# Optimization experiments

Hardware: AMD Instinct MI355X
Metric: run time of the kernel (lower is better)

Reference implementation:

```python
import jax, jax.numpy as jnp
import numpy as np

N = 100000   # total nodes
E = 1000000  # edges
D = 64       # input_dim
H = 128      # embed_dim


def setup_inputs() -> dict:
    key = jax.random.key(0)
    k1, k2, k3, k4 = jax.random.split(key, 4)
    nodes = jnp.arange(N, dtype=jnp.int32)
    features = jax.random.normal(k1, (N, D), dtype=jnp.float32)
    edge_index = jax.random.randint(k2, (2, E), 0, N, dtype=jnp.int32)
    # nn.Linear(2*D, H): weight [H, 2D], bias [H]
    W = jax.random.normal(k3, (H, 2 * D), dtype=jnp.float32) / np.sqrt(2 * D)
    b = jax.random.normal(k4, (H,), dtype=jnp.float32) * 0.01
    return {"nodes": nodes, "features": features, "edge_index": edge_index,
            "W": W, "b": b}


def reference(nodes, features, edge_index, W, b):
    src, dst = edge_index[0], edge_index[1]
    # gcn=False: neighbors are undirected (both src->dst and dst->src).
    # Mean aggregator over all neighbors (full-neighborhood mean).
    ones = jnp.ones((E,), dtype=features.dtype)
    neigh_sum = (jax.ops.segment_sum(features[dst], src, num_segments=N)
                 + jax.ops.segment_sum(features[src], dst, num_segments=N))
    deg = (jax.ops.segment_sum(ones, src, num_segments=N)
           + jax.ops.segment_sum(ones, dst, num_segments=N))
    neigh_mean = neigh_sum / jnp.maximum(deg, 1.0)[:, None]  # [N, D]
    self_feats = features[nodes]            # [B, D]
    neigh_feats = neigh_mean[nodes]         # [B, D]
    combined = jnp.concatenate([self_feats, neigh_feats], axis=1)  # [B, 2D]
    out = jax.nn.relu(combined @ W.T + b)   # [B, H]
    return out
```

## Files before the change

### kernel.cpp

```cpp
#include <hip/hip_runtime.h>
#include <hip/hip_bf16.h>


#define D_IN 64
#define H_OUT 128
#define CAP 64
#define CAP_L 61
#define NPB 32
#define BSHIFT 7
#define BUK_N 128
#define NBUK_MAX 1024
#define PASSA_BLOCKS 256
#define PASSA_THREADS 512

typedef unsigned long long ull;
typedef unsigned short ushortt;
typedef unsigned char uchar;
typedef __attribute__((ext_vector_type(8))) short bf16x8;
typedef __attribute__((ext_vector_type(4))) float f32x4;
typedef __attribute__((ext_vector_type(2))) float f32x2;

__device__ __forceinline__ ushortt f2bf(float f) {
    __hip_bfloat16 h = __float2bfloat16(f);
    return *reinterpret_cast<ushortt*>(&h);
}
__device__ __forceinline__ float bf2f(ushortt u) {
    unsigned int x = ((unsigned int)u) << 16;
    return __uint_as_float(x);
}

__global__ __launch_bounds__(PASSA_THREADS) void prep_kernel(
    const int* __restrict__ ei,
    unsigned* __restrict__ gbuf,
    int* __restrict__ blkcnt,
    const float4* __restrict__ feat4,
    const float4* __restrict__ w4,
    ushortt* __restrict__ fb,
    uint2* __restrict__ fq,
    ushortt* __restrict__ Wb,
    int E, int nbuk, int scap, int chunk, int nfeat8, int nw8)
{
    const int t = threadIdx.x;

    if (blockIdx.x >= PASSA_BLOCKS) {
        int i = (blockIdx.x - PASSA_BLOCKS) * PASSA_THREADS + t;
        if (i < nfeat8) {
            float4 a = feat4[2 * i], b = feat4[2 * i + 1];
            bf16x8 o;
            o[0] = (short)f2bf(a.x); o[1] = (short)f2bf(a.y);
            o[2] = (short)f2bf(a.z); o[3] = (short)f2bf(a.w);
            o[4] = (short)f2bf(b.x); o[5] = (short)f2bf(b.y);
            o[6] = (short)f2bf(b.z); o[7] = (short)f2bf(b.w);
            *(bf16x8*)&fb[(size_t)i * 8] = o;
            unsigned lo = (unsigned)__builtin_amdgcn_cvt_pk_fp8_f32(a.x, a.y, 0, false);
            lo = (unsigned)__builtin_amdgcn_cvt_pk_fp8_f32(a.z, a.w, (int)lo, true);
            unsigned hi = (unsigned)__builtin_amdgcn_cvt_pk_fp8_f32(b.x, b.y, 0, false);
            hi = (unsigned)__builtin_amdgcn_cvt_pk_fp8_f32(b.z, b.w, (int)hi, true);
            uint2 q; q.x = lo; q.y = hi;
            fq[i] = q;
        } else {
            int j = i - nfeat8;
            if (j < nw8) {
                float4 a = w4[2 * j], b = w4[2 * j + 1];
                bf16x8 o;
                o[0] = (short)f2bf(a.x); o[1] = (short)f2bf(a.y);
                o[2] = (short)f2bf(a.z); o[3] = (short)f2bf(a.w);
                o[4] = (short)f2bf(b.x); o[5] = (short)f2bf(b.y);
                o[6] = (short)f2bf(b.z); o[7] = (short)f2bf(b.w);
                *(bf16x8*)&Wb[(size_t)j * 8] = o;
            }
        }
        return;
    }

    __shared__ int lcnt[NBUK_MAX];
    for (int i = t; i < nbuk; i += PASSA_THREADS) lcnt[i] = 0;
    __syncthreads();

    const int E2 = 2 * E;
    int lo = blockIdx.x * chunk;
    int hi = lo + chunk; if (hi > E2) hi = E2;

    for (int i = lo + t; i < hi; i += PASSA_THREADS) {
        int u = ei[i];
        int v = (i < E) ? ei[E + i] : ei[i - E];
        int b = u >> BSHIFT;
        unsigned pk = ((unsigned)v << BSHIFT) | (unsigned)(u & (BUK_N - 1));
        int p = atomicAdd(&lcnt[b], 1);
        if (p < scap) gbuf[((size_t)blockIdx.x * nbuk + b) * scap + p] = pk;
    }
    __syncthreads();
    for (int b = t; b < nbuk; b += PASSA_THREADS)
        blkcnt[blockIdx.x * nbuk + b] = lcnt[b];
}

__global__ __launch_bounds__(512, 8) void adj_agg_kernel(
    const unsigned* __restrict__ gbuf,
    const int* __restrict__ blkcnt,
    const int* __restrict__ ei,
    const uchar* __restrict__ fq,
    ushortt* __restrict__ meanb,
    int N, int E, int nbuk, int scap)
{
    __shared__ unsigned adj_l[BUK_N * CAP_L];
    __shared__ int cnt_l[BUK_N];
    __shared__ int scnt_l[PASSA_BLOCKS];
    __shared__ int satf;

    const int b = blockIdx.x;
    const int t = threadIdx.x;

    if (t == 0) satf = 0;
    if (t < BUK_N) cnt_l[t] = 0;
    if (t < PASSA_BLOCKS) {
        int c = blkcnt[t * nbuk + b];
        scnt_l[t] = c;
        if (c > scap) satf = 1;
    }
    __syncthreads();

    const int wv   = t >> 6;
    const int lane = t & 63;

    if (satf) {
        const int E2 = 2 * E;
        for (int i = t; i < E2; i += 512) {
            int u = ei[i];
            if ((u >> BSHIFT) != b) continue;
            int v = (i < E) ? ei[E + i] : ei[i - E];
            int ul = u & (BUK_N - 1);
            int p  = atomicAdd(&cnt_l[ul], 1);
            if (p < CAP_L) adj_l[ul * CAP_L + p] = (unsigned)v;
        }
    } else {
        for (int seg = wv; seg < PASSA_BLOCKS; seg += 8) {
            int c = scnt_l[seg]; if (c > scap) c = scap;
            const unsigned* base = gbuf + ((size_t)seg * nbuk + b) * scap;
            for (int i = lane; i < c; i += 64) {
                unsigned e = base[i];
                int ul = e & (BUK_N - 1);
                int v  = (int)(e >> BSHIFT);
                int p  = atomicAdd(&cnt_l[ul], 1);
                if (p < CAP_L) adj_l[ul * CAP_L + p] = (unsigned)v;
            }
        }
    }
    __syncthreads();

    const int oct = lane >> 3;
    const int ol  = lane & 7;
    const uchar* fqb = fq + ol * 8;

    const int nbase = wv * 16;
    const int gbase = (b << BSHIFT) + nbase;

#define GATHER(U0, U1, U2, U3, AROW, CC)                                     \
    {                                                                        \
        if ((CC) > 0) {                                                      \
            int jj = oct;      int a = jj < (CC);                            \
            unsigned id = (AROW)[a ? jj : 0];                                \
            U0 = *(const uint2*)(fqb + (size_t)(id * 64u));                  \
            if (!a) { U0.x = 0u; U0.y = 0u; }                                \
        } else { U0.x = 0u; U0.y = 0u; }                                     \
        if ((CC) > 8) {                                                      \
            int jj = 8 + oct;  int a = jj < (CC);                            \
            unsigned id = (AROW)[a ? jj : 0];                                \
            U1 = *(const uint2*)(fqb + (size_t)(id * 64u));                  \
            if (!a) { U1.x = 0u; U1.y = 0u; }                                \
        } else { U1.x = 0u; U1.y = 0u; }                                     \
        if ((CC) > 16) {                                                     \
            int jj = 16 + oct; int a = jj < (CC);                            \
            unsigned id = (AROW)[a ? jj : 0];                                \
            U2 = *(const uint2*)(fqb + (size_t)(id * 64u));                  \
            if (!a) { U2.x = 0u; U2.y = 0u; }                                \
        } else { U2.x = 0u; U2.y = 0u; }                                     \
        if ((CC) > 24) {                                                     \
            int jj = 24 + oct; int a = jj < (CC);                            \
            unsigned id = (AROW)[a ? jj : 0];                                \
            U3 = *(const uint2*)(fqb + (size_t)(id * 64u));                  \
            if (!a) { U3.x = 0u; U3.y = 0u; }                                \
        } else { U3.x = 0u; U3.y = 0u; }                                     \
    }

#define DEC(u)                                                       \
    s0 += __builtin_amdgcn_cvt_pk_f32_fp8((int)(u).x, false);        \
    s1 += __builtin_amdgcn_cvt_pk_f32_fp8((int)(u).x, true);         \
    s2 += __builtin_amdgcn_cvt_pk_f32_fp8((int)(u).y, false);        \
    s3 += __builtin_amdgcn_cvt_pk_f32_fp8((int)(u).y, true);

    uint2 cu0, cu1, cu2, cu3;
    uint2 nu0, nu1, nu2, nu3;

    int c_cur = 0, cc_cur = 0;
    {
        if (gbase < N) c_cur = cnt_l[nbase];
        cc_cur = c_cur < CAP_L ? c_cur : CAP_L;
        const unsigned* arow = &adj_l[nbase * CAP_L];
        GATHER(cu0, cu1, cu2, cu3, arow, cc_cur);
    }

    for (int ni = 0; ni < 16; ++ni) {
        const int n = nbase + ni;
        const int g = gbase + ni;

        int c_nxt = 0, cc_nxt = 0;
        if (ni < 15) {
            if (g + 1 < N) c_nxt = cnt_l[n + 1];
            cc_nxt = c_nxt < CAP_L ? c_nxt : CAP_L;
            const unsigned* arown = &adj_l[(n + 1) * CAP_L];
            GATHER(nu0, nu1, nu2, nu3, arown, cc_nxt);
        }

        if (g < N) {
            f32x2 s0 = {0.f, 0.f}, s1 = {0.f, 0.f};
            f32x2 s2 = {0.f, 0.f}, s3 = {0.f, 0.f};
            DEC(cu0); DEC(cu1); DEC(cu2); DEC(cu3);

            if (__builtin_expect(cc_cur > 32, 0)) {
                const unsigned* arow = &adj_l[n * CAP_L];
                for (int j = 32; j < cc_cur; j += 8) {
                    int jj = j + oct; int a = jj < cc_cur;
                    unsigned id = arow[a ? jj : 0];
                    uint2 u = *(const uint2*)(fqb + (size_t)(id * 64u));
                    if (!a) { u.x = 0u; u.y = 0u; }
                    DEC(u);
                }
            }

            f32x2 a0, a1;
            {
                f32x2 t0, t1, t2, t3;
                t0.x = __shfl_xor(s0.x, 8);  t0.y = __shfl_xor(s0.y, 8);
                t1.x = __shfl_xor(s1.x, 8);  t1.y = __shfl_xor(s1.y, 8);
                t2.x = __shfl_xor(s2.x, 8);  t2.y = __shfl_xor(s2.y, 8);
                t3.x = __shfl_xor(s3.x, 8);  t3.y = __shfl_xor(s3.y, 8);
                bool hi = (oct & 1);
                a0 = hi ? (s2 + t2) : (s0 + t0);
                a1 = hi ? (s3 + t3) : (s1 + t1);
            }
            f32x2 b0;
            {
                f32x2 t0, t1;
                t0.x = __shfl_xor(a0.x, 16); t0.y = __shfl_xor(a0.y, 16);
                t1.x = __shfl_xor(a1.x, 16); t1.y = __shfl_xor(a1.y, 16);
                bool hi = (oct & 2);
                b0 = hi ? (a1 + t1) : (a0 + t0);
            }
            float cf;
            {
                f32x2 tt;
                tt.x = __shfl_xor(b0.x, 32); tt.y = __shfl_xor(b0.y, 32);
                f32x2 ss = b0 + tt;
                cf = (oct & 4) ? ss.y : ss.x;
            }

            float r = 1.0f / fmaxf((float)c_cur, 1.0f);
            int d = 8 * ol + 4 * (oct & 1) + (oct & 2) + ((oct >> 2) & 1);
            meanb[(size_t)g * D_IN + d] = f2bf(cf * r);
        }

        c_cur = c_nxt; cc_cur = cc_nxt;
        cu0 = nu0; cu1 = nu1; cu2 = nu2; cu3 = nu3;
    }
#undef GATHER
#undef DEC
}

__global__ __launch_bounds__(256) void build_adj_kernel(
    const int* __restrict__ ei,
    int* __restrict__ cnt,
    int* __restrict__ adj,
    int E)
{
    const int part   = blockIdx.x & 7;
    const int bloc   = blockIdx.x >> 3;
    const int nbp    = gridDim.x >> 3;
    const int stride = nbp * 256;
    const int E2     = 2 * E;

    for (int i = bloc * 256 + (int)threadIdx.x; i < E2; i += stride) {
        int u = ei[i];
        if (((u >> 4) & 7) != part) continue;
        int v = (i < E) ? ei[E + i] : ei[i - E];
        int p = atomicAdd(&cnt[u], 1);
        if (p < CAP_L) adj[u * CAP + p] = v;
    }
}

__global__ __launch_bounds__(256) void aggregate_f32_kernel(
    const float* __restrict__ feat,
    const int* __restrict__ adj,
    const int* __restrict__ cnt,
    ushortt* __restrict__ meanb,
    int N)
{
    int wid  = (blockIdx.x * blockDim.x + threadIdx.x) >> 6;
    int lane = threadIdx.x & 63;
    if (wid >= N) return;

    int c  = cnt[wid];
    int cc = c < CAP_L ? c : CAP_L;
    int ids = adj[wid * CAP + lane];

    float sum = 0.0f;
    int j = 0;
    for (; j + 8 <= cc; j += 8) {
        int i0 = __shfl(ids, j + 0);
        int i1 = __shfl(ids, j + 1);
        int i2 = __shfl(ids, j + 2);
        int i3 = __shfl(ids, j + 3);
        int i4 = __shfl(ids, j + 4);
        int i5 = __shfl(ids, j + 5);
        int i6 = __shfl(ids, j + 6);
        int i7 = __shfl(ids, j + 7);
        float f0 = feat[i0 * D_IN + lane];
        float f1 = feat[i1 * D_IN + lane];
        float f2 = feat[i2 * D_IN + lane];
        float f3 = feat[i3 * D_IN + lane];
        float f4 = feat[i4 * D_IN + lane];
        float f5 = feat[i5 * D_IN + lane];
        float f6 = feat[i6 * D_IN + lane];
        float f7 = feat[i7 * D_IN + lane];
        sum += ((f0 + f1) + (f2 + f3)) + ((f4 + f5) + (f6 + f7));
    }
    for (; j < cc; ++j)
        sum += feat[__shfl(ids, j) * D_IN + lane];

    float m = sum / fmaxf((float)c, 1.0f);
    meanb[(size_t)wid * D_IN + lane] = f2bf(m);
}

__global__ __launch_bounds__(256) void gemm_mfma_kernel(
    const int* __restrict__ nodes,
    const ushortt* __restrict__ fb,
    const ushortt* __restrict__ meanb,
    const ushortt* __restrict__ Wb,
    const float* __restrict__ bias,
    float* __restrict__ out,
    int N)
{
    __shared__ ushortt w_lds[128 * 136];
    __shared__ int gnode[64];

    const int t  = threadIdx.x;
    const int n0 = blockIdx.x * 64;

    if (t < 64) {
        int idx = n0 + t;
        gnode[t] = nodes[idx < N ? idx : N - 1];
    }
    for (int i = t; i < 128 * 16; i += 256) {
        int row = i >> 4, seg = i & 15;
        *(bf16x8*)&w_lds[row * 136 + seg * 8] =
            *(const bf16x8*)&Wb[row * 128 + seg * 8];
    }
    __syncthreads();

    const int w    = t >> 6;
    const int lane = t & 63;
    const int l15  = lane & 15;
    const int quad = lane >> 4;

    const int g = gnode[w * 16 + l15];
    const bf16x8 a0 = *(const bf16x8*)&fb[(size_t)g * D_IN +  0 + quad * 8];
    const bf16x8 a1 = *(const bf16x8*)&fb[(size_t)g * D_IN + 32 + quad * 8];
    const bf16x8 a2 = *(const bf16x8*)&meanb[(size_t)g * D_IN +  0 + quad * 8];
    const bf16x8 a3 = *(const bf16x8*)&meanb[(size_t)g * D_IN + 32 + quad * 8];

    const int  out_row = n0 + w * 16 + l15;
    const bool valid   = out_row < N;

#pragma unroll
    for (int tile = 0; tile < 8; ++tile) {
        const int h0 = tile * 16;
        const ushortt* wrow = &w_lds[(h0 + l15) * 136];
        bf16x8 b0 = *(const bf16x8*)&wrow[ 0 + quad * 8];
        bf16x8 b1 = *(const bf16x8*)&wrow[32 + quad * 8];
        bf16x8 b2 = *(const bf16x8*)&wrow[64 + quad * 8];
        bf16x8 b3 = *(const bf16x8*)&wrow[96 + quad * 8];

        f32x4 acc = {0.f, 0.f, 0.f, 0.f};
        acc = __builtin_amdgcn_mfma_f32_16x16x32_bf16(b0, a0, acc, 0, 0, 0);
        acc = __builtin_amdgcn_mfma_f32_16x16x32_bf16(b1, a1, acc, 0, 0, 0);
        acc = __builtin_amdgcn_mfma_f32_16x16x32_bf16(b2, a2, acc, 0, 0, 0);
        acc = __builtin_amdgcn_mfma_f32_16x16x32_bf16(b3, a3, acc, 0, 0, 0);

        if (valid) {
            float4 bv = *(const float4*)&bias[h0 + quad * 4];
            float4 o;
            o.x = fmaxf(acc[0] + bv.x, 0.0f);
            o.y = fmaxf(acc[1] + bv.y, 0.0f);
            o.z = fmaxf(acc[2] + bv.z, 0.0f);
            o.w = fmaxf(acc[3] + bv.w, 0.0f);
            *(float4*)&out[(size_t)out_row * H_OUT + h0 + quad * 4] = o;
        }
    }
}

__global__ __launch_bounds__(256) void gemm_kernel(
    const int* __restrict__ nodes,
    const float* __restrict__ feat,
    const ushortt* __restrict__ meanb,
    const float* __restrict__ W,
    const float* __restrict__ bias,
    float* __restrict__ out,
    int N)
{
    __shared__ float w_lds[64 * 132];
    __shared__ float comb_self[NPB * 68];
    __shared__ float comb_mean[NPB * 68];
    __shared__ int   gnode[NPB];

    const int t  = threadIdx.x;
    const int n0 = blockIdx.x * NPB;

    if (t < NPB) {
        int idx = n0 + t;
        if (idx >= N) idx = N - 1;
        gnode[t] = nodes[idx];
    }
    __syncthreads();

    for (int i = t; i < NPB * 64; i += 256) {
        int n = i >> 6, d = i & 63;
        int g = gnode[n];
        comb_self[n * 68 + d] = feat[g * D_IN + d];
        comb_mean[n * 68 + d] = bf2f(meanb[(size_t)g * D_IN + d]);
    }
    for (int i = t; i < H_OUT * 64; i += 256) {
        int h = i >> 6, kk = i & 63;
        w_lds[kk * 132 + h] = W[h * (2 * D_IN) + kk];
    }
    __syncthreads();

    const int tx = t & 31;
    const int ty = t >> 5;
    const int h0 = tx * 4;
    const int nl = ty * 4;

    float acc[4][4];
#pragma unroll
    for (int j = 0; j < 4; j++)
#pragma unroll
        for (int i = 0; i < 4; i++) acc[j][i] = 0.0f;

    for (int kk = 0; kk < 64; kk += 4) {
        float4 wvv[4], cv[4];
#pragma unroll
        for (int i = 0; i < 4; i++)
            wvv[i] = *(const float4*)&w_lds[(kk + i) * 132 + h0];
#pragma unroll
        for (int j = 0; j < 4; j++)
            cv[j] = *(const float4*)&comb_self[(nl + j) * 68 + kk];
#pragma unroll
        for (int j = 0; j < 4; j++) {
            const float* c = (const float*)&cv[j];
#pragma unroll
            for (int i = 0; i < 4; i++) {
                const float* wp = (const float*)&wvv[i];
                acc[j][0] += wp[0] * c[i];
                acc[j][1] += wp[1] * c[i];
                acc[j][2] += wp[2] * c[i];
                acc[j][3] += wp[3] * c[i];
            }
        }
    }
    __syncthreads();

    for (int i = t; i < H_OUT * 64; i += 256) {
        int h = i >> 6, kk = i & 63;
        w_lds[kk * 132 + h] = W[h * (2 * D_IN) + 64 + kk];
    }
    __syncthreads();

    for (int kk = 0; kk < 64; kk += 4) {
        float4 wvv[4], cv[4];
#pragma unroll
        for (int i = 0; i < 4; i++)
            wvv[i] = *(const float4*)&w_lds[(kk + i) * 132 + h0];
#pragma unroll
        for (int j = 0; j < 4; j++)
            cv[j] = *(const float4*)&comb_mean[(nl + j) * 68 + kk];
#pragma unroll
        for (int j = 0; j < 4; j++) {
            const float* c = (const float*)&cv[j];
#pragma unroll
            for (int i = 0; i < 4; i++) {
                const float* wp = (const float*)&wvv[i];
                acc[j][0] += wp[0] * c[i];
                acc[j][1] += wp[1] * c[i];
                acc[j][2] += wp[2] * c[i];
                acc[j][3] += wp[3] * c[i];
            }
        }
    }

    float4 bv = *(const float4*)&bias[h0];
#pragma unroll
    for (int j = 0; j < 4; j++) {
        int n = n0 + nl + j;
        if (n >= N) continue;
        float4 o;
        o.x = fmaxf(acc[j][0] + bv.x, 0.0f);
        o.y = fmaxf(acc[j][1] + bv.y, 0.0f);
        o.z = fmaxf(acc[j][2] + bv.z, 0.0f);
        o.w = fmaxf(acc[j][3] + bv.w, 0.0f);
        *(float4*)&out[(size_t)n * H_OUT + h0] = o;
    }
}

extern "C" void kernel_launch(void* const* d_in, const int* in_sizes, int n_in,
                              void* d_out, int out_size, void* d_ws, size_t ws_size,
                              hipStream_t stream) {
    const int*   nodes = (const int*)d_in[0];
    const float* feat  = (const float*)d_in[1];
    const int*   ei    = (const int*)d_in[2];
    const float* W     = (const float*)d_in[3];
    const float* bias  = (const float*)d_in[4];
    float*       out   = (float*)d_out;

    const int N  = in_sizes[0];
    const int E  = in_sizes[2] / 2;
    const int E2 = 2 * E;

    const int nbuk  = (N + BUK_N - 1) >> BSHIFT;
    const int chunk = (E2 + PASSA_BLOCKS - 1) / PASSA_BLOCKS;
    double ex = (double)chunk * (double)BUK_N / (double)N;
    int scap = ((int)(ex + 9.0 * __builtin_sqrt(ex)) + 31) & ~15;
    if (scap < 64) scap = 64;

    char* base = (char*)d_ws;
    size_t off = 0;
    auto aln = [](size_t x) { return (x + 63) & ~(size_t)63; };
    int*     cnt    = (int*)(base + off);     off = aln(off + (size_t)N * 4);
    int*     adj    = (int*)(base + off);     off = aln(off + (size_t)N * CAP * 4);
    ushortt* meanb  = (ushortt*)(base + off); off = aln(off + (size_t)N * D_IN * 2);
    int*     blkcnt = (int*)(base + off);     off = aln(off + (size_t)PASSA_BLOCKS * NBUK_MAX * 4);
    ushortt* Wb     = (ushortt*)(base + off); off = aln(off + (size_t)H_OUT * 2 * D_IN * 2);
    ushortt* fb     = (ushortt*)(base + off); off = aln(off + (size_t)N * D_IN * 2);
    uchar*   fq     = (uchar*)(base + off);   off = aln(off + (size_t)N * D_IN);
    unsigned* gbuf  = (unsigned*)(base + off);
    const size_t total = off + (size_t)PASSA_BLOCKS * nbuk * scap * 4;

    const bool full = (N <= 131072) && (nbuk <= NBUK_MAX) && (ws_size >= total)
                   && ((N * D_IN) % 8 == 0);

    if (full) {
        const int nfeat8 = N * D_IN / 8;
        const int nw8    = H_OUT * 2 * D_IN / 8;
        const int conv_blocks = (nfeat8 + nw8 + PASSA_THREADS - 1) / PASSA_THREADS;
        prep_kernel<<<PASSA_BLOCKS + conv_blocks, PASSA_THREADS, 0, stream>>>(
            ei, gbuf, blkcnt, (const float4*)feat, (const float4*)W,
            fb, (uint2*)fq, Wb, E, nbuk, scap, chunk, nfeat8, nw8);
        adj_agg_kernel<<<nbuk, 512, 0, stream>>>(gbuf, blkcnt, ei, fq,
                                                 meanb, N, E, nbuk, scap);
        gemm_mfma_kernel<<<(N + 63) / 64, 256, 0, stream>>>(
            nodes, fb, meanb, Wb, bias, out, N);
    } else {
        const int ablocks = (int)(((size_t)N * 64 + 255) / 256);
        hipMemsetAsync(cnt, 0, (size_t)N * sizeof(int), stream);
        build_adj_kernel<<<2048, 256, 0, stream>>>(ei, cnt, adj, E);
        aggregate_f32_kernel<<<ablocks, 256, 0, stream>>>(feat, adj, cnt,
                                                          meanb, N);
        gemm_kernel<<<(N + NPB - 1) / NPB, 256, 0, stream>>>(
            nodes, feat, meanb, W, bias, out, N);
    }
}
```

Measured before the change: 192.3 us.

## Double node bucket size, use 1024-thread aggregation blocks, gather two nodes per step

Node buckets grow from 128 to 256 nodes, which halves the bucket count. The adjacency/aggregation kernel now runs with 1024 threads per block, so each block stages twice as many adjacency lists in LDS. The one-ahead software-pipelined gather loop is replaced by a loop that issues fp8 feature gathers for two nodes before reducing either, aiming for more memory-level parallelism per wave. The cost is that each block needs close to 64KB of LDS and there are fewer, larger blocks, which can hurt occupancy and load balance across CUs.

```diff
diff --git a/kernel.cpp b/kernel.cpp
--- a/kernel.cpp
+++ b/kernel.cpp
@@ -7,9 +7,9 @@
 #define CAP 64
 #define CAP_L 61
 #define NPB 32
-#define BSHIFT 7
-#define BUK_N 128
-#define NBUK_MAX 1024
+#define BSHIFT 8
+#define BUK_N 256
+#define NBUK_MAX 512
 #define PASSA_BLOCKS 256
 #define PASSA_THREADS 512
 
@@ -94,7 +94,7 @@
         blkcnt[blockIdx.x * nbuk + b] = lcnt[b];
 }
 
-__global__ __launch_bounds__(512, 8) void adj_agg_kernel(
+__global__ __launch_bounds__(1024) void adj_agg_kernel(
     const unsigned* __restrict__ gbuf,
     const int* __restrict__ blkcnt,
     const int* __restrict__ ei,
@@ -124,7 +124,7 @@
 
     if (satf) {
         const int E2 = 2 * E;
-        for (int i = t; i < E2; i += 512) {
+        for (int i = t; i < E2; i += 1024) {
             int u = ei[i];
             if ((u >> BSHIFT) != b) continue;
             int v = (i < E) ? ei[E + i] : ei[i - E];
@@ -133,7 +133,7 @@
             if (p < CAP_L) adj_l[ul * CAP_L + p] = (unsigned)v;
         }
     } else {
-        for (int seg = wv; seg < PASSA_BLOCKS; seg += 8) {
+        for (int seg = wv; seg < PASSA_BLOCKS; seg += 16) {
             int c = scnt_l[seg]; if (c > scap) c = scap;
             const unsigned* base = gbuf + ((size_t)seg * nbuk + b) * scap;
             for (int i = lane; i < c; i += 64) {
@@ -154,32 +154,32 @@
     const int nbase = wv * 16;
     const int gbase = (b << BSHIFT) + nbase;
 
-#define GATHER(U0, U1, U2, U3, AROW, CC)                                     \
+#define GATH(U0, U1, U2, U3, AROW, CC)                                       \
     {                                                                        \
         if ((CC) > 0) {                                                      \
             int jj = oct;      int a = jj < (CC);                            \
             unsigned id = (AROW)[a ? jj : 0];                                \
             U0 = *(const uint2*)(fqb + (size_t)(id * 64u));                  \
             if (!a) { U0.x = 0u; U0.y = 0u; }                                \
-        } else { U0.x = 0u; U0.y = 0u; }                                     \
+        }                                                                    \
         if ((CC) > 8) {                                                      \
             int jj = 8 + oct;  int a = jj < (CC);                            \
             unsigned id = (AROW)[a ? jj : 0];                                \
             U1 = *(const uint2*)(fqb + (size_t)(id * 64u));                  \
             if (!a) { U1.x = 0u; U1.y = 0u; }                                \
-        } else { U1.x = 0u; U1.y = 0u; }                                     \
+        }                                                                    \
         if ((CC) > 16) {                                                     \
             int jj = 16 + oct; int a = jj < (CC);                            \
             unsigned id = (AROW)[a ? jj : 0];                                \
             U2 = *(const uint2*)(fqb + (size_t)(id * 64u));                  \
             if (!a) { U2.x = 0u; U2.y = 0u; }                                \
-        } else { U2.x = 0u; U2.y = 0u; }                                     \
+        }                                                                    \
         if ((CC) > 24) {                                                     \
             int jj = 24 + oct; int a = jj < (CC);                            \
             unsigned id = (AROW)[a ? jj : 0];                                \
             U3 = *(const uint2*)(fqb + (size_t)(id * 64u));                  \
             if (!a) { U3.x = 0u; U3.y = 0u; }                                \
-        } else { U3.x = 0u; U3.y = 0u; }                                     \
+        }                                                                    \
     }
 
 #define DEC(u)                                                       \
@@ -188,82 +188,74 @@
     s2 += __builtin_amdgcn_cvt_pk_f32_fp8((int)(u).y, false);        \
     s3 += __builtin_amdgcn_cvt_pk_f32_fp8((int)(u).y, true);
 
-    uint2 cu0, cu1, cu2, cu3;
-    uint2 nu0, nu1, nu2, nu3;
-
-    int c_cur = 0, cc_cur = 0;
-    {
-        if (gbase < N) c_cur = cnt_l[nbase];
-        cc_cur = c_cur < CAP_L ? c_cur : CAP_L;
-        const unsigned* arow = &adj_l[nbase * CAP_L];
-        GATHER(cu0, cu1, cu2, cu3, arow, cc_cur);
-    }
-
-    for (int ni = 0; ni < 16; ++ni) {
-        const int n = nbase + ni;
-        const int g = gbase + ni;
-
-        int c_nxt = 0, cc_nxt = 0;
-        if (ni < 15) {
-            if (g + 1 < N) c_nxt = cnt_l[n + 1];
-            cc_nxt = c_nxt < CAP_L ? c_nxt : CAP_L;
-            const unsigned* arown = &adj_l[(n + 1) * CAP_L];
-            GATHER(nu0, nu1, nu2, nu3, arown, cc_nxt);
-        }
-
-        if (g < N) {
-            f32x2 s0 = {0.f, 0.f}, s1 = {0.f, 0.f};
-            f32x2 s2 = {0.f, 0.f}, s3 = {0.f, 0.f};
-            DEC(cu0); DEC(cu1); DEC(cu2); DEC(cu3);
-
-            if (__builtin_expect(cc_cur > 32, 0)) {
-                const unsigned* arow = &adj_l[n * CAP_L];
-                for (int j = 32; j < cc_cur; j += 8) {
-                    int jj = j + oct; int a = jj < cc_cur;
-                    unsigned id = arow[a ? jj : 0];
-                    uint2 u = *(const uint2*)(fqb + (size_t)(id * 64u));
-                    if (!a) { u.x = 0u; u.y = 0u; }
-                    DEC(u);
-                }
-            }
-
-            f32x2 a0, a1;
-            {
-                f32x2 t0, t1, t2, t3;
-                t0.x = __shfl_xor(s0.x, 8);  t0.y = __shfl_xor(s0.y, 8);
-                t1.x = __shfl_xor(s1.x, 8);  t1.y = __shfl_xor(s1.y, 8);
-                t2.x = __shfl_xor(s2.x, 8);  t2.y = __shfl_xor(s2.y, 8);
-                t3.x = __shfl_xor(s3.x, 8);  t3.y = __shfl_xor(s3.y, 8);
-                bool hi = (oct & 1);
-                a0 = hi ? (s2 + t2) : (s0 + t0);
-                a1 = hi ? (s3 + t3) : (s1 + t1);
-            }
-            f32x2 b0;
-            {
-                f32x2 t0, t1;
-                t0.x = __shfl_xor(a0.x, 16); t0.y = __shfl_xor(a0.y, 16);
-                t1.x = __shfl_xor(a1.x, 16); t1.y = __shfl_xor(a1.y, 16);
-                bool hi = (oct & 2);
-                b0 = hi ? (a1 + t1) : (a0 + t0);
-            }
-            float cf;
-            {
-                f32x2 tt;
-                tt.x = __shfl_xor(b0.x, 32); tt.y = __shfl_xor(b0.y, 32);
-                f32x2 ss = b0 + tt;
-                cf = (oct & 4) ? ss.y : ss.x;
-            }
-
-            float r = 1.0f / fmaxf((float)c_cur, 1.0f);
-            int d = 8 * ol + 4 * (oct & 1) + (oct & 2) + ((oct >> 2) & 1);
-            meanb[(size_t)g * D_IN + d] = f2bf(cf * r);
-        }
-
-        c_cur = c_nxt; cc_cur = cc_nxt;
-        cu0 = nu0; cu1 = nu1; cu2 = nu2; cu3 = nu3;
-    }
-#undef GATHER
+#define FINISH(UA, UB, UC, UD, CC, CTRUE, AROW, G)                           \
+    {                                                                        \
+        f32x2 s0 = {0.f, 0.f}, s1 = {0.f, 0.f};                              \
+        f32x2 s2 = {0.f, 0.f}, s3 = {0.f, 0.f};                              \
+        DEC(UA); DEC(UB); DEC(UC); DEC(UD);                                  \
+        if (__builtin_expect((CC) > 32, 0)) {                                \
+            for (int j = 32; j < (CC); j += 8) {                             \
+                int jj = j + oct; int a = jj < (CC);                         \
+                unsigned id = (AROW)[a ? jj : 0];                            \
+                uint2 u = *(const uint2*)(fqb + (size_t)(id * 64u));         \
+                if (!a) { u.x = 0u; u.y = 0u; }                              \
+                DEC(u);                                                      \
+            }                                                                \
+        }                                                                    \
+        f32x2 a0, a1;                                                        \
+        {                                                                    \
+            f32x2 t0, t1, t2, t3;                                            \
+            t0.x = __shfl_xor(s0.x, 8);  t0.y = __shfl_xor(s0.y, 8);         \
+            t1.x = __shfl_xor(s1.x, 8);  t1.y = __shfl_xor(s1.y, 8);         \
+            t2.x = __shfl_xor(s2.x, 8);  t2.y = __shfl_xor(s2.y, 8);         \
+            t3.x = __shfl_xor(s3.x, 8);  t3.y = __shfl_xor(s3.y, 8);         \
+            bool hi = (oct & 1);                                             \
+            a0 = hi ? (s2 + t2) : (s0 + t0);                                 \
+            a1 = hi ? (s3 + t3) : (s1 + t1);                                 \
+        }                                                                    \
+        f32x2 b0;                                                            \
+        {                                                                    \
+            f32x2 t0, t1;                                                    \
+            t0.x = __shfl_xor(a0.x, 16); t0.y = __shfl_xor(a0.y, 16);        \
+            t1.x = __shfl_xor(a1.x, 16); t1.y = __shfl_xor(a1.y, 16);        \
+            bool hi = (oct & 2);                                             \
+            b0 = hi ? (a1 + t1) : (a0 + t0);                                 \
+        }                                                                    \
+        float cf;                                                            \
+        {                                                                    \
+            f32x2 tt;                                                        \
+            tt.x = __shfl_xor(b0.x, 32); tt.y = __shfl_xor(b0.y, 32);        \
+            f32x2 ss = b0 + tt;                                              \
+            cf = (oct & 4) ? ss.y : ss.x;                                    \
+        }                                                                    \
+        float r = 1.0f / fmaxf((float)(CTRUE), 1.0f);                        \
+        int d = 8 * ol + 4 * (oct & 1) + (oct & 2) + ((oct >> 2) & 1);       \
+        meanb[(size_t)(G) * D_IN + d] = f2bf(cf * r);                        \
+    }
+
+    for (int np = 0; np < 8; ++np) {
+        const int n0 = nbase + 2 * np;
+        const int g0 = gbase + 2 * np;
+        const int g1 = g0 + 1;
+
+        const int c0  = (g0 < N) ? cnt_l[n0] : 0;
+        const int c1  = (g1 < N) ? cnt_l[n0 + 1] : 0;
+        const int cc0 = c0 < CAP_L ? c0 : CAP_L;
+        const int cc1 = c1 < CAP_L ? c1 : CAP_L;
+        const unsigned* ar0 = &adj_l[n0 * CAP_L];
+        const unsigned* ar1 = &adj_l[(n0 + 1) * CAP_L];
+
+        uint2 u00 = {0u,0u}, u01 = {0u,0u}, u02 = {0u,0u}, u03 = {0u,0u};
+        uint2 u10 = {0u,0u}, u11 = {0u,0u}, u12 = {0u,0u}, u13 = {0u,0u};
+        GATH(u00, u01, u02, u03, ar0, cc0);
+        GATH(u10, u11, u12, u13, ar1, cc1);
+
+        if (g0 < N) FINISH(u00, u01, u02, u03, cc0, c0, ar0, g0);
+        if (g1 < N) FINISH(u10, u11, u12, u13, cc1, c1, ar1, g1);
+    }
+#undef GATH
 #undef DEC
+#undef FINISH
 }
 
 __global__ __launch_bounds__(256) void build_adj_kernel(
@@ -552,8 +544,8 @@
         prep_kernel<<<PASSA_BLOCKS + conv_blocks, PASSA_THREADS, 0, stream>>>(
             ei, gbuf, blkcnt, (const float4*)feat, (const float4*)W,
             fb, (uint2*)fq, Wb, E, nbuk, scap, chunk, nfeat8, nw8);
-        adj_agg_kernel<<<nbuk, 512, 0, stream>>>(gbuf, blkcnt, ei, fq,
-                                                 meanb, N, E, nbuk, scap);
+        adj_agg_kernel<<<nbuk, 1024, 0, stream>>>(gbuf, blkcnt, ei, fq,
+                                                  meanb, N, E, nbuk, scap);
         gemm_mfma_kernel<<<(N + 63) / 64, 256, 0, stream>>>(
             nodes, fb, meanb, Wb, bias, out, N);
     } else {
```

Result: faster. 169.9 us (-11.7%).
